# Kernel tuning notes

Hardware: AMD Instinct MI355X
Metric: run time of the kernel (lower is better)

The kernel has to match this reference:

```python
import jax, jax.numpy as jnp
import numpy as np
from jax import lax

B, N_CELL, N_NODE, E, H = 512, 12, 40, 128, 128
CLIP = 10.0
NEG = -1e9


def _ptr_logits(query, target, mask, Wq, bq, Wk, bk, v):
    # query [B,E], target [B,N,E], mask [B,N] (1 = visited)
    u = jnp.einsum('bnh,h->bn', jnp.tanh((query @ Wq + bq)[:, None, :] + target @ Wk + bk), v)
    return jnp.where(mask > 0, NEG, CLIP * jnp.tanh(u))


def _forward(node_context, cell_context, original_data, high_mask, low_mask,
             init_w, W_hc, b_hc, W_vw, b_vw, Wq, bq, Wk, bk, v,
             low_init_w, low_W_hc, low_b_hc, low_W_vw, low_b_vw,
             low_Wq, low_bq, low_Wk, low_bk, low_v):
    ar = jnp.arange(B)
    root = jax.random.key(42)
    high_keys = jax.random.split(jax.random.fold_in(root, 0), N_CELL)
    low_keys = jax.random.split(jax.random.fold_in(root, 1), N_CELL)

    def low_decode(cell_emb, cell_coords, key):
        # cell_emb [B,n_node,E], cell_coords [B,n_node,2]
        h_bar = jnp.mean(cell_emb, 1) @ low_W_hc + low_b_hc
        q0 = h_bar + low_init_w @ low_W_vw + low_b_vw

        def step(carry, k):
            query, mask, init_h, i = carry
            logits = _ptr_logits(query, cell_emb, mask, low_Wq, low_bq, low_Wk, low_bk, low_v)
            idx = jax.random.categorical(k, logits)            # [B]
            lp = jnp.take_along_axis(jax.nn.log_softmax(logits, -1), idx[:, None], 1)[:, 0]
            mask = mask.at[ar, idx].set(1.0)
            h = cell_emb[ar, idx]
            coord = cell_coords[ar, idx]
            init_h = jnp.where(i == 0, h, init_h)
            query = h_bar + jnp.concatenate([init_h, h], -1) @ low_W_vw + low_b_vw
            return (query, mask, init_h, i + 1), (idx, lp, coord)

        keys = jax.random.split(key, N_NODE)
        carry0 = (q0, low_mask, jnp.zeros_like(h_bar), jnp.int32(0))
        _, (idxs, lps, coords) = lax.scan(step, carry0, keys)
        # tour length inside the cell
        reward = jnp.sum(jnp.linalg.norm(coords[1:] - coords[:-1], axis=-1), 0)  # [B]
        return lps.sum(0), idxs.T, reward, coords[0], coords[-1]

    h_bar = jnp.mean(cell_context, 1) @ W_hc + b_hc
    q0 = h_bar + init_w @ W_vw + b_vw

    def step(carry, ks):
        query, mask, init_h, last_node, i = carry
        k_hi, k_lo = ks
        logits = _ptr_logits(query, cell_context, mask, Wq, bq, Wk, bk, v)
        idx = jax.random.categorical(k_hi, logits)             # [B]
        clp = jnp.take_along_axis(jax.nn.log_softmax(logits, -1), idx[:, None], 1)[:, 0]
        cur_emb = node_context[ar, idx]                        # [B,n_node,E]
        cur_coords = original_data[ar, idx]                    # [B,n_node,2]
        llp, lact, lrew, init_node, new_last = low_decode(cur_emb, cur_coords, k_lo)
        # distance from previous cell's last node to this cell's first node (i>0 only)
        crew = jnp.where(i > 0, jnp.linalg.norm(init_node - last_node, axis=1), 0.0)
        mask = mask.at[ar, idx].set(1.0)
        h = cell_context[ar, idx]
        init_h = jnp.where(i == 0, h, init_h)
        query = h_bar + jnp.concatenate([init_h, h], -1) @ W_vw + b_vw
        return (query, mask, init_h, new_last, i + 1), (idx, clp, crew, llp, lact, lrew)

    carry0 = (q0, high_mask, jnp.zeros_like(h_bar), jnp.zeros((B, 2), jnp.float32), jnp.int32(0))
    _, (idxs, clps, crews, llps, lacts, lrews) = lax.scan(step, carry0, (high_keys, low_keys))

    cell_log_prob = clps.sum(0)                                # [B]
    cell_action = idxs.T                                       # [B, n_cell]
    cell_reward = crews.sum(0)                                 # [B] (i==0 term is 0)
    node_log_prob = llps.T.reshape(-1, 1)                      # [B*n_cell, 1]
    node_action = jnp.transpose(lacts, (1, 0, 2)).reshape(-1, N_NODE)
    node_reward = lrews.T.reshape(-1, 1)
    return cell_log_prob, node_log_prob, cell_reward, node_reward, cell_action, node_action


def setup_inputs() -> dict:
    key = jax.random.key(0)
    ks = jax.random.split(key, 32)

    def lin(k, fan_in, shape):
        b = 1.0 / np.sqrt(fan_in)
        return jax.random.uniform(k, shape, jnp.float32, -b, b)

    return {
        'node_context': jax.random.normal(ks[0], (B, N_CELL, N_NODE, E), jnp.float32),
        'cell_context': jax.random.normal(ks[1], (B, N_CELL, E), jnp.float32),
        'original_data': jax.random.uniform(ks[2], (B, N_CELL, N_NODE, 2), jnp.float32),
        'high_mask': jnp.zeros((B, N_CELL), jnp.float32),
        'low_mask': jnp.zeros((B, N_NODE), jnp.float32),
        'init_w': jax.random.uniform(ks[3], (2 * E,), jnp.float32, -1.0, 1.0),
        'W_hc': lin(ks[4], E, (E, E)), 'b_hc': lin(ks[5], E, (E,)),
        'W_vw': lin(ks[6], 2 * E, (2 * E, E)), 'b_vw': lin(ks[7], 2 * E, (E,)),
        'Wq': lin(ks[8], E, (E, H)), 'bq': lin(ks[9], E, (H,)),
        'Wk': lin(ks[10], E, (E, H)), 'bk': lin(ks[11], E, (H,)),
        'v': lin(ks[12], H, (H,)),
        'low_init_w': jax.random.uniform(ks[13], (2 * E,), jnp.float32, -1.0, 1.0),
        'low_W_hc': lin(ks[14], E, (E, E)), 'low_b_hc': lin(ks[15], E, (E,)),
        'low_W_vw': lin(ks[16], 2 * E, (2 * E, E)), 'low_b_vw': lin(ks[17], 2 * E, (E,)),
        'low_Wq': lin(ks[18], E, (E, H)), 'low_bq': lin(ks[19], E, (H,)),
        'low_Wk': lin(ks[20], E, (E, H)), 'low_bk': lin(ks[21], E, (H,)),
        'low_v': lin(ks[22], H, (H,)),
    }


def reference(node_context, cell_context, original_data, high_mask, low_mask,
              init_w, W_hc, b_hc, W_vw, b_vw, Wq, bq, Wk, bk, v,
              low_init_w, low_W_hc, low_b_hc, low_W_vw, low_b_vw,
              low_Wq, low_bq, low_Wk, low_bk, low_v):
    return _forward(node_context, cell_context, original_data, high_mask, low_mask,
                    init_w, W_hc, b_hc, W_vw, b_vw, Wq, bq, Wk, bk, v,
                    low_init_w, low_W_hc, low_b_hc, low_W_vw, low_b_vw,
                    low_Wq, low_bq, low_Wk, low_bk, low_v)
```

## Files before the change

kernel.cpp:

```cpp
#include <hip/hip_runtime.h>
#include <stdint.h>


#define NB    512
#define NCELL 12
#define NNODE 40
#define EDIM  128
#define EDP   129
#define THREADS 256

#define OFF_CLP  0
#define OFF_NLP  512
#define OFF_CRW  6656
#define OFF_NRW  7168
#define OFF_CACT 13312
#define OFF_NACT 19456

#define WS_PTS_BASE   6144
#define WS_META_BASE  30720
#define WS_U_BASE     55296
#define WS_GUM_BASE   9885696
#define WS_TOTAL_F    19716096ull

__device__ __forceinline__ uint32_t rotl32(uint32_t x, int d) {
  return (x << d) | (x >> (32 - d));
}

__device__ __forceinline__ void tf2x32(uint32_t k0, uint32_t k1,
                                       uint32_t c0, uint32_t c1,
                                       uint32_t& o0, uint32_t& o1) {
  uint32_t ks2 = k0 ^ k1 ^ 0x1BD11BDAu;
  uint32_t x0 = c0 + k0, x1 = c1 + k1;
#define TFR(r) { x0 += x1; x1 = rotl32(x1, (r)); x1 ^= x0; }
  TFR(13) TFR(15) TFR(26) TFR(6)   x0 += k1;  x1 += ks2 + 1u;
  TFR(17) TFR(29) TFR(16) TFR(24)  x0 += ks2; x1 += k0 + 2u;
  TFR(13) TFR(15) TFR(26) TFR(6)   x0 += k0;  x1 += k1 + 3u;
  TFR(17) TFR(29) TFR(16) TFR(24)  x0 += k1;  x1 += ks2 + 4u;
  TFR(13) TFR(15) TFR(26) TFR(6)   x0 += ks2; x1 += k0 + 5u;
#undef TFR
  o0 = x0; o1 = x1;
}

__device__ __forceinline__ uint32_t draw_bits(uint32_t k0, uint32_t k1,
                                              uint32_t idx) {
  uint32_t o0, o1;
  tf2x32(k0, k1, 0u, idx, o0, o1);
  return o0 ^ o1;
}

__device__ __forceinline__ float bits_to_gumbel(uint32_t bits) {
  uint32_t fb = (bits >> 9) | 0x3F800000u;
  float f = __uint_as_float(fb) - 1.0f;
  const float TINY = 1.17549435082228751e-38f;
  float u = f * (1.0f - TINY) + TINY;
  u = fmaxf(TINY, u);
  return -logf(-logf(u));
}

__device__ __forceinline__ float xla_tanh(float x) {
#pragma clang fp contract(off)
  float ax = fabsf(x);
  float xc = fminf(fmaxf(x, -9.0f), 9.0f);
  float x2 = xc * xc;
  float nm = -2.76076847742355e-16f;
  nm = nm * x2 + 2.00018790482477e-13f;
  nm = nm * x2 + -8.60467152213735e-11f;
  nm = nm * x2 + 5.12229709037114e-08f;
  nm = nm * x2 + 1.48572235717979e-05f;
  nm = nm * x2 + 6.37261928875436e-04f;
  nm = nm * x2 + 4.89352455891786e-03f;
  nm = xc * nm;
  float dn = 1.19825839466702e-06f;
  dn = dn * x2 + 1.18534705686654e-04f;
  dn = dn * x2 + 2.26843463243900e-03f;
  dn = dn * x2 + 4.89352518554385e-03f;
  return (ax < 0.0004f) ? x : (nm / dn);
}

template<int KLEN>
__device__ __forceinline__ void matvec(const float* __restrict__ W,
                                       const float* __restrict__ src,
                                       const float* __restrict__ pre,
                                       const float* __restrict__ bias,
                                       float* dest, float* part, int t) {
  const int j  = t & 127;
  const int hv = t >> 7;
  const int kh = KLEN / 2;
  const int k0 = hv * kh;
  float acc = 0.f;
  const float* Wp = W + (size_t)k0 * EDIM + j;
  const float* sp = src + k0;
#pragma unroll 8
  for (int k = 0; k < kh; ++k) acc = fmaf(sp[k], Wp[(size_t)k * EDIM], acc);
  if (hv) part[j] = acc;
  __syncthreads();
  if (!hv) {
    float r = acc + part[j];
    if (pre)  r += pre[j];
    if (bias) r += bias[j];
    dest[j] = r;
  }
  __syncthreads();
}

template<int RPH, int SSTR, int DSTR>
__device__ __forceinline__ void computeK(const float* __restrict__ W,
                                         const float* __restrict__ bias,
                                         const float* src, float* dst, int t) {
  const int j  = t & 127;
  const int hv = t >> 7;
  float acc[RPH];
#pragma unroll
  for (int s = 0; s < RPH; ++s) acc[s] = 0.f;
  const float* Wp = W + j;
#pragma unroll 4
  for (int k = 0; k < EDIM; ++k) {
    float w = Wp[(size_t)k * EDIM];
#pragma unroll
    for (int s = 0; s < RPH; ++s)
      acc[s] = fmaf(src[(hv + 2 * s) * SSTR + k], w, acc[s]);
  }
  float bj = bias[j];
#pragma unroll
  for (int s = 0; s < RPH; ++s) dst[(hv + 2 * s) * DSTR + j] = acc[s] + bj;
}

__global__ __launch_bounds__(THREADS, 2)
void high_kernel(const float* __restrict__ cell_context,
                 const float* __restrict__ high_mask,
                 const float* __restrict__ init_w,
                 const float* __restrict__ W_hc,  const float* __restrict__ b_hc,
                 const float* __restrict__ W_vw,  const float* __restrict__ b_vw,
                 const float* __restrict__ Wq,    const float* __restrict__ bq,
                 const float* __restrict__ Wk,    const float* __restrict__ bk,
                 const float* __restrict__ v_hi,
                 float* __restrict__ out, int* __restrict__ ws_cidx) {
  const int b = blockIdx.x;
  const int t = threadIdx.x;

  __shared__ float s_cc[NCELL][EDIM];
  __shared__ float s_Kh[NCELL][EDIM];
  __shared__ float s_ghum[NCELL * NCELL];
  __shared__ float s_qh[EDIM], s_qq[EDIM], s_qbh[EDIM], s_hbh[EDIM];
  __shared__ float s_mean[EDIM], s_part[EDIM];
  __shared__ float s_vh[EDIM], s_bqh[EDIM];
  __shared__ float s_iw[2 * EDIM];
  __shared__ float s_u[NCELL];
  __shared__ float s_maskh[NCELL];
  __shared__ uint32_t s_kh[NCELL][2];
  __shared__ uint32_t s_base[2];
  __shared__ int s_idx;

  if (t == 0) {
    uint32_t a0, a1;
    tf2x32(0u, 42u, 0u, 0u, a0, a1); s_base[0] = a0; s_base[1] = a1;
  }
  __syncthreads();
  if (t < NCELL)
    tf2x32(s_base[0], s_base[1], 0u, (uint32_t)t, s_kh[t][0], s_kh[t][1]);

  if (t < EDIM) { s_vh[t] = v_hi[t]; s_bqh[t] = bq[t]; }
  s_iw[t] = init_w[t];
  if (t < NCELL) s_maskh[t] = high_mask[b * NCELL + t];

  if (t < EDIM) {
    float s = 0.f;
    for (int n = 0; n < NCELL; ++n) {
      float x = cell_context[((size_t)b * NCELL + n) * EDIM + t];
      s_cc[n][t] = x; s += x;
    }
    s_mean[t] = s / 12.0f;
  }
  __syncthreads();
  if (t < NCELL * NCELL) {
    int ci = t / NCELL, n = t - ci * NCELL;
    s_ghum[t] = bits_to_gumbel(draw_bits(s_kh[ci][0], s_kh[ci][1],
                                         (uint32_t)(b * NCELL + n)));
  }
  matvec<128>(W_hc, s_mean, nullptr, b_hc, s_hbh, s_part, t);
  computeK<6, EDIM, EDIM>(Wk, bk, &s_cc[0][0], &s_Kh[0][0], t);
  __syncthreads();
  matvec<256>(W_vw, s_iw, s_hbh, b_vw, s_qh, s_part, t);
  if (t < EDIM) s_qbh[t] = s_hbh[t] + b_vw[t];
  __syncthreads();

  float cell_lp = 0.f;

  for (int ci = 0; ci < NCELL; ++ci) {
    matvec<128>(Wq, s_qh, nullptr, s_bqh, s_qq, s_part, t);
    if (t < 4 * NCELL) {
      int nd = t >> 2, p = t & 3, rot = t & 31;
      float acc = 0.f;
#pragma unroll 4
      for (int i2 = 0; i2 < 32; ++i2) {
        int h = p * 32 + ((i2 + rot) & 31);
        acc = fmaf(s_vh[h], xla_tanh(s_qq[h] + s_Kh[nd][h]), acc);
      }
      acc += __shfl_xor(acc, 1);
      acc += __shfl_xor(acc, 2);
      if (p == 0) s_u[nd] = acc;
    }
    __syncthreads();

    if (t < 64) {
      float logit = -__builtin_huge_valf(), val = -__builtin_huge_valf();
      if (t < NCELL) {
        float lg = (s_maskh[t] > 0.f) ? -1e9f : 10.0f * xla_tanh(s_u[t]);
        logit = lg;
        val = lg + s_ghum[ci * NCELL + t];
      }
      int bidx = t;
      float mx = logit;
#pragma unroll
      for (int d = 32; d; d >>= 1) {
        float oval = __shfl_xor(val, d);
        int   oidx = __shfl_xor(bidx, d);
        float omx  = __shfl_xor(mx, d);
        if (oval > val || (oval == val && oidx < bidx)) { val = oval; bidx = oidx; }
        mx = fmaxf(mx, omx);
      }
      float ex = (t < NCELL) ? expf(logit - mx) : 0.f;
#pragma unroll
      for (int d = 32; d; d >>= 1) ex += __shfl_xor(ex, d);
      float chosen = __shfl(logit, bidx);
      cell_lp += (chosen - mx) - logf(ex);
      if (t == 0) {
        s_idx = bidx;
        s_maskh[bidx] = 1.0f;
        out[OFF_CACT + b * NCELL + ci] = (float)bidx;
        ws_cidx[b * NCELL + ci] = bidx;
      }
    }
    __syncthreads();
    const int cidx = s_idx;

    if (ci == 0)
      matvec<128>(W_vw, &s_cc[cidx][0], s_qbh, nullptr, s_qbh, s_part, t);
    if (ci < NCELL - 1)
      matvec<128>(W_vw + 128 * EDIM, &s_cc[cidx][0], s_qbh, nullptr, s_qh, s_part, t);
  }

  if (t == 0) out[OFF_CLP + b] = cell_lp;
}

__global__ __launch_bounds__(THREADS, 3)
void low_pre_kernel(const float* __restrict__ node_context,
                    const float* __restrict__ original_data,
                    const float* __restrict__ low_mask,
                    const float* __restrict__ low_init_w,
                    const float* __restrict__ low_W_hc, const float* __restrict__ low_b_hc,
                    const float* __restrict__ low_W_vw, const float* __restrict__ low_b_vw,
                    const float* __restrict__ low_Wq,   const float* __restrict__ low_bq,
                    const float* __restrict__ low_Wk,   const float* __restrict__ low_bk,
                    const float* __restrict__ v_lo,
                    const int* __restrict__ ws_cidx,
                    float* __restrict__ ws_meta,
                    float* __restrict__ ws_U,
                    float* __restrict__ ws_gum,
                    float* __restrict__ out) {
  const int bc = blockIdx.x;
  const int b  = bc / NCELL;
  const int ci = bc - b * NCELL;
  const int t  = threadIdx.x;
  const int j  = t & 127;
  const int hv = t >> 7;

  __shared__ float s_eq[NNODE * EDP];
  __shared__ float s_Kl[NNODE * EDP];
  __shared__ float s_g0[NNODE];
  __shared__ float s_coords[NNODE][2];
  __shared__ float s_ql[EDIM], s_qq[EDIM], s_qbl[EDIM], s_hbl[EDIM];
  __shared__ float s_mean[EDIM], s_part[EDIM];
  __shared__ float s_vl[EDIM], s_bql[EDIM];
  __shared__ float s_iwl[2 * EDIM];
  __shared__ float s_u[NNODE];
  __shared__ float s_maskl[NNODE];
  __shared__ uint32_t s_ks[NNODE][2];
  __shared__ uint32_t s_kk[2];
  __shared__ int s_cidx;
  __shared__ int s_idx;

  if (t == 0) {
    uint32_t a0, a1, c0, c1;
    tf2x32(0u, 42u, 0u, 1u, a0, a1);
    tf2x32(a0, a1, 0u, (uint32_t)ci, c0, c1);
    s_kk[0] = c0; s_kk[1] = c1;
    s_cidx = ws_cidx[bc];
  }
  __syncthreads();
  const int cidx = s_cidx;

  if (t < EDIM) { s_vl[t] = v_lo[t]; s_bql[t] = low_bq[t]; }
  s_iwl[t] = low_init_w[t];
  if (t < NNODE)
    tf2x32(s_kk[0], s_kk[1], 0u, (uint32_t)t, s_ks[t][0], s_ks[t][1]);

  const float* embg = node_context + (((size_t)b * NCELL + cidx) * NNODE) * EDIM;
  if (t < EDIM) {
    float s = 0.f;
    for (int n = 0; n < NNODE; ++n) {
      float x = embg[n * EDIM + t];
      s_eq[n * EDP + t] = x; s += x;
    }
    s_mean[t] = s / 40.0f;
  }
  if (t >= 128 && t < 208) {
    int q = t - 128;
    s_coords[q >> 1][q & 1] = original_data[(((size_t)b * NCELL + cidx) * NNODE) * 2 + q];
  }
  if (t >= 208 && t < 208 + NNODE) s_maskl[t - 208] = low_mask[b * NNODE + (t - 208)];
  __syncthreads();

  {
    float* gg = ws_gum + (size_t)bc * (NNODE * NNODE);
    for (int g = t; g < NNODE * NNODE; g += THREADS) {
      int st = g / NNODE, n = g - st * NNODE;
      float gv = bits_to_gumbel(draw_bits(s_ks[st][0], s_ks[st][1],
                                          (uint32_t)(b * NNODE + n)));
      gg[g] = gv;
      if (g < NNODE) s_g0[g] = gv;
    }
  }
  matvec<128>(low_W_hc, s_mean, nullptr, low_b_hc, s_hbl, s_part, t);
  computeK<20, EDP, EDP>(low_Wk, low_bk, &s_eq[0], &s_Kl[0], t);

  {
    float accA[20], accB[20];
#pragma unroll
    for (int s = 0; s < 20; ++s) { accA[s] = 0.f; accB[s] = 0.f; }
    const float* Wb = low_W_vw + (size_t)128 * EDIM + j;
#pragma unroll 2
    for (int k = 0; k < 64; ++k) {
      float w = Wb[(size_t)k * EDIM];
#pragma unroll
      for (int s = 0; s < 20; ++s)
        accA[s] = fmaf(s_eq[(hv + 2 * s) * EDP + k], w, accA[s]);
    }
#pragma unroll 2
    for (int k = 64; k < 128; ++k) {
      float w = Wb[(size_t)k * EDIM];
#pragma unroll
      for (int s = 0; s < 20; ++s)
        accB[s] = fmaf(s_eq[(hv + 2 * s) * EDP + k], w, accB[s]);
    }
    __syncthreads();
#pragma unroll
    for (int s = 0; s < 20; ++s)
      s_eq[(hv + 2 * s) * EDP + j] = accA[s] + accB[s];
  }
  matvec<256>(low_W_vw, s_iwl, s_hbl, low_b_vw, s_ql, s_part, t);
  if (t < EDIM) s_qbl[t] = s_hbl[t] + low_b_vw[t];
  __syncthreads();

  matvec<128>(low_Wq, s_ql, nullptr, s_bql, s_qq, s_part, t);
  if (t < 160) {
    int nd = t >> 2, p = t & 3, rot = t & 31;
    float acc = 0.f;
#pragma unroll 4
    for (int i2 = 0; i2 < 32; ++i2) {
      int h = p * 32 + ((i2 + rot) & 31);
      acc = fmaf(s_vl[h], xla_tanh(s_qq[h] + s_Kl[nd * EDP + h]), acc);
    }
    acc += __shfl_xor(acc, 1);
    acc += __shfl_xor(acc, 2);
    if (p == 0) s_u[nd] = acc;
  }
  __syncthreads();

  if (t < 64) {
    float maskreg = (t < NNODE) ? s_maskl[t] : 1.0f;
    float logit = -__builtin_huge_valf(), val = -__builtin_huge_valf();
    if (t < NNODE) {
      float lg = (maskreg > 0.f) ? -1e9f : 10.0f * xla_tanh(s_u[t]);
      logit = lg;
      val = lg + s_g0[t];
    }
    int bidx = t;
    float mx = logit;
#pragma unroll
    for (int d = 32; d; d >>= 1) {
      float oval = __shfl_xor(val, d);
      int   oidx = __shfl_xor(bidx, d);
      float omx  = __shfl_xor(mx, d);
      if (oval > val || (oval == val && oidx < bidx)) { val = oval; bidx = oidx; }
      mx = fmaxf(mx, omx);
    }
    float ex = (t < NNODE) ? expf(logit - mx) : 0.f;
#pragma unroll
    for (int d = 32; d; d >>= 1) ex += __shfl_xor(ex, d);
    float chosen = __shfl(logit, bidx);
    float lp0 = (chosen - mx) - logf(ex);
    if (t == 0) {
      s_idx = bidx;
      out[OFF_NACT + ((size_t)bc) * NNODE + 0] = (float)bidx;
      float4 m; m.x = s_coords[bidx][0]; m.y = s_coords[bidx][1];
      m.z = lp0; m.w = (float)bidx;
      reinterpret_cast<float4*>(ws_meta)[bc] = m;
    }
  }
  __syncthreads();

  {
    const int n0 = s_idx;
    matvec<128>(low_W_vw, embg + (size_t)n0 * EDIM, s_qbl, nullptr, s_qbl, s_part, t);
    for (int i = t; i < NNODE * EDIM; i += THREADS) {
      int n = i >> 7, k = i & 127;
      s_eq[n * EDP + k] = s_eq[n * EDP + k] + s_qbl[k];
    }
    __syncthreads();
    {
      float ac0[20], ac1[20];
#pragma unroll
      for (int s = 0; s < 20; ++s) { ac0[s] = 0.f; ac1[s] = 0.f; }
      const float* Wqp = low_Wq + (size_t)(hv * 64) * EDIM + j;
      const float* qlb = &s_eq[0] + hv * 64;
#pragma unroll 2
      for (int k = 0; k < 64; ++k) {
        float w = Wqp[(size_t)k * EDIM];
#pragma unroll
        for (int s = 0; s < 20; ++s)
          ac0[s] = fmaf(qlb[s * EDP + k], w, ac0[s]);
#pragma unroll
        for (int s = 0; s < 20; ++s)
          ac1[s] = fmaf(qlb[(20 + s) * EDP + k], w, ac1[s]);
      }
      __syncthreads();
      if (hv) {
#pragma unroll
        for (int s = 0; s < 20; ++s) {
          s_eq[s * EDP + j]        = ac0[s];
          s_eq[(20 + s) * EDP + j] = ac1[s];
        }
      }
      __syncthreads();
      if (!hv) {
#pragma unroll
        for (int s = 0; s < 20; ++s) {
          s_eq[s * EDP + j]        = (ac0[s] + s_eq[s * EDP + j])        + s_bql[j];
          s_eq[(20 + s) * EDP + j] = (ac1[s] + s_eq[(20 + s) * EDP + j]) + s_bql[j];
        }
      }
      __syncthreads();
    }
  }

  {
    float* wU = ws_U + (size_t)bc * (NNODE * NNODE);
    for (int e = t; e < NNODE * NNODE; e += THREADS) {
      int nd = e / NNODE, prow = e - nd * NNODE;
      const float* qr = &s_eq[prow * EDP];
      const float* kr = &s_Kl[nd * EDP];
      float S[4];
#pragma unroll
      for (int p = 0; p < 4; ++p) {
        int rot = (4 * nd + p) & 31;
        float a = 0.f;
#pragma unroll 4
        for (int i2 = 0; i2 < 32; ++i2) {
          int h = p * 32 + ((i2 + rot) & 31);
          a = fmaf(s_vl[h], xla_tanh(qr[h] + kr[h]), a);
        }
        S[p] = a;
      }
      wU[prow * NNODE + nd] = (S[0] + S[1]) + (S[2] + S[3]);
    }
  }
}

__global__ __launch_bounds__(64)
void low_tail_kernel(const float* __restrict__ original_data,
                     const float* __restrict__ low_mask,
                     const int* __restrict__ ws_cidx,
                     const float* __restrict__ ws_meta,
                     const float* __restrict__ ws_U,
                     const float* __restrict__ ws_gum,
                     float* __restrict__ ws_pts,
                     float* __restrict__ out) {
  const int bc = blockIdx.x;
  const int b  = bc / NCELL;
  const int t  = threadIdx.x;

  __shared__ float sU[NNODE * NNODE];
  __shared__ float sG[NNODE * NNODE];
  __shared__ float sc[NNODE][2];
  __shared__ int s_cidx;

  if (t == 0) s_cidx = ws_cidx[bc];
  __syncthreads();
  const int cidx = s_cidx;

  {
    const float4* u4 = reinterpret_cast<const float4*>(ws_U + (size_t)bc * 1600);
    const float4* g4 = reinterpret_cast<const float4*>(ws_gum + (size_t)bc * 1600);
    float4* su4 = reinterpret_cast<float4*>(sU);
    float4* sg4 = reinterpret_cast<float4*>(sG);
    for (int i = t; i < 400; i += 64) { su4[i] = u4[i]; sg4[i] = g4[i]; }
    for (int q = t; q < 80; q += 64)
      sc[q >> 1][q & 1] = original_data[(((size_t)b * NCELL + cidx) * NNODE) * 2 + q];
  }
  float4 meta = reinterpret_cast<const float4*>(ws_meta)[bc];
  int   prev  = (int)meta.w;
  float initx = meta.x, inity = meta.y;
  float llp   = meta.z;
  float prevx = initx, prevy = inity, rew = 0.f;
  float maskreg = (t < NNODE) ? low_mask[b * NNODE + t] : 1.0f;
  if (t == prev) maskreg = 1.0f;
  __syncthreads();

  for (int st = 1; st < NNODE; ++st) {
    float logit = -__builtin_huge_valf(), val = -__builtin_huge_valf();
    if (t < NNODE) {
      float lg = (maskreg > 0.f) ? -1e9f : 10.0f * xla_tanh(sU[prev * NNODE + t]);
      logit = lg;
      val = lg + sG[st * NNODE + t];
    }
    int bidx = t;
    float mx = logit;
#pragma unroll
    for (int d = 32; d; d >>= 1) {
      float oval = __shfl_xor(val, d);
      int   oidx = __shfl_xor(bidx, d);
      float omx  = __shfl_xor(mx, d);
      if (oval > val || (oval == val && oidx < bidx)) { val = oval; bidx = oidx; }
      mx = fmaxf(mx, omx);
    }
    float ex = (t < NNODE) ? expf(logit - mx) : 0.f;
#pragma unroll
    for (int d = 32; d; d >>= 1) ex += __shfl_xor(ex, d);
    float chosen = __shfl(logit, bidx);
    llp += (chosen - mx) - logf(ex);
    float cx = sc[bidx][0], cy = sc[bidx][1];
    { float dx = cx - prevx, dy = cy - prevy; rew += sqrtf(dx * dx + dy * dy); }
    prevx = cx; prevy = cy;
    if (t == bidx) maskreg = 1.0f;
    prev = bidx;
    if (t == 0)
      out[OFF_NACT + ((size_t)bc) * NNODE + st] = (float)bidx;
  }
  if (t == 0) {
    out[OFF_NLP + bc] = llp;
    out[OFF_NRW + bc] = rew;
    float* p = ws_pts + (size_t)bc * 4;
    p[0] = initx; p[1] = inity; p[2] = prevx; p[3] = prevy;
  }
}

__global__ __launch_bounds__(THREADS, 2)
void low_kernel_fused(const float* __restrict__ node_context,
                      const float* __restrict__ original_data,
                      const float* __restrict__ low_mask,
                      const float* __restrict__ low_init_w,
                      const float* __restrict__ low_W_hc, const float* __restrict__ low_b_hc,
                      const float* __restrict__ low_W_vw, const float* __restrict__ low_b_vw,
                      const float* __restrict__ low_Wq,   const float* __restrict__ low_bq,
                      const float* __restrict__ low_Wk,   const float* __restrict__ low_bk,
                      const float* __restrict__ v_lo,
                      const int* __restrict__ ws_cidx,
                      float* __restrict__ ws_pts,
                      float* __restrict__ out) {
  const int bc = blockIdx.x;
  const int b  = bc / NCELL;
  const int ci = bc - b * NCELL;
  const int t  = threadIdx.x;
  const int j  = t & 127;
  const int hv = t >> 7;

  __shared__ float s_eq[NNODE * EDP];
  __shared__ float s_Kl[NNODE * EDP];
  __shared__ float s_U[NNODE * NNODE];
  __shared__ float s_gum[NNODE * NNODE];
  __shared__ float s_coords[NNODE][2];
  __shared__ float s_ql[EDIM], s_qq[EDIM], s_qbl[EDIM], s_hbl[EDIM];
  __shared__ float s_mean[EDIM], s_part[EDIM];
  __shared__ float s_vl[EDIM], s_bql[EDIM];
  __shared__ float s_iwl[2 * EDIM];
  __shared__ float s_u[NNODE];
  __shared__ float s_maskl[NNODE];
  __shared__ uint32_t s_ks[NNODE][2];
  __shared__ uint32_t s_kk[2];
  __shared__ int s_cidx;
  __shared__ int s_idx;

  if (t == 0) {
    uint32_t a0, a1, c0, c1;
    tf2x32(0u, 42u, 0u, 1u, a0, a1);
    tf2x32(a0, a1, 0u, (uint32_t)ci, c0, c1);
    s_kk[0] = c0; s_kk[1] = c1;
    s_cidx = ws_cidx[bc];
  }
  __syncthreads();
  const int cidx = s_cidx;

  if (t < EDIM) { s_vl[t] = v_lo[t]; s_bql[t] = low_bq[t]; }
  s_iwl[t] = low_init_w[t];
  if (t < NNODE)
    tf2x32(s_kk[0], s_kk[1], 0u, (uint32_t)t, s_ks[t][0], s_ks[t][1]);

  const float* embg = node_context + (((size_t)b * NCELL + cidx) * NNODE) * EDIM;
  if (t < EDIM) {
    float s = 0.f;
    for (int n = 0; n < NNODE; ++n) {
      float x = embg[n * EDIM + t];
      s_eq[n * EDP + t] = x; s += x;
    }
    s_mean[t] = s / 40.0f;
  }
  if (t >= 128 && t < 208) {
    int q = t - 128;
    s_coords[q >> 1][q & 1] = original_data[(((size_t)b * NCELL + cidx) * NNODE) * 2 + q];
  }
  if (t >= 208 && t < 208 + NNODE) s_maskl[t - 208] = low_mask[b * NNODE + (t - 208)];
  __syncthreads();

  for (int g = t; g < NNODE * NNODE; g += THREADS) {
    int st = g / NNODE, n = g - st * NNODE;
    s_gum[g] = bits_to_gumbel(draw_bits(s_ks[st][0], s_ks[st][1],
                                        (uint32_t)(b * NNODE + n)));
  }
  matvec<128>(low_W_hc, s_mean, nullptr, low_b_hc, s_hbl, s_part, t);
  computeK<20, EDP, EDP>(low_Wk, low_bk, &s_eq[0], &s_Kl[0], t);

  {
    float accA[20], accB[20];
#pragma unroll
    for (int s = 0; s < 20; ++s) { accA[s] = 0.f; accB[s] = 0.f; }
    const float* Wb = low_W_vw + (size_t)128 * EDIM + j;
#pragma unroll 2
    for (int k = 0; k < 64; ++k) {
      float w = Wb[(size_t)k * EDIM];
#pragma unroll
      for (int s = 0; s < 20; ++s)
        accA[s] = fmaf(s_eq[(hv + 2 * s) * EDP + k], w, accA[s]);
    }
#pragma unroll 2
    for (int k = 64; k < 128; ++k) {
      float w = Wb[(size_t)k * EDIM];
#pragma unroll
      for (int s = 0; s < 20; ++s)
        accB[s] = fmaf(s_eq[(hv + 2 * s) * EDP + k], w, accB[s]);
    }
    __syncthreads();
#pragma unroll
    for (int s = 0; s < 20; ++s)
      s_eq[(hv + 2 * s) * EDP + j] = accA[s] + accB[s];
  }
  matvec<256>(low_W_vw, s_iwl, s_hbl, low_b_vw, s_ql, s_part, t);
  if (t < EDIM) s_qbl[t] = s_hbl[t] + low_b_vw[t];
  __syncthreads();

  matvec<128>(low_Wq, s_ql, nullptr, s_bql, s_qq, s_part, t);
  if (t < 160) {
    int nd = t >> 2, p = t & 3, rot = t & 31;
    float acc = 0.f;
#pragma unroll 4
    for (int i2 = 0; i2 < 32; ++i2) {
      int h = p * 32 + ((i2 + rot) & 31);
      acc = fmaf(s_vl[h], xla_tanh(s_qq[h] + s_Kl[nd * EDP + h]), acc);
    }
    acc += __shfl_xor(acc, 1);
    acc += __shfl_xor(acc, 2);
    if (p == 0) s_u[nd] = acc;
  }
  __syncthreads();

  float llp = 0.f, rew = 0.f, prevx = 0.f, prevy = 0.f, initx = 0.f, inity = 0.f;
  float maskreg = 1.0f;
  int prev = 0;
  if (t < 64) {
    maskreg = (t < NNODE) ? s_maskl[t] : 1.0f;
    float logit = -__builtin_huge_valf(), val = -__builtin_huge_valf();
    if (t < NNODE) {
      float lg = (maskreg > 0.f) ? -1e9f : 10.0f * xla_tanh(s_u[t]);
      logit = lg;
      val = lg + s_gum[t];
    }
    int bidx = t;
    float mx = logit;
#pragma unroll
    for (int d = 32; d; d >>= 1) {
      float oval = __shfl_xor(val, d);
      int   oidx = __shfl_xor(bidx, d);
      float omx  = __shfl_xor(mx, d);
      if (oval > val || (oval == val && oidx < bidx)) { val = oval; bidx = oidx; }
      mx = fmaxf(mx, omx);
    }
    float ex = (t < NNODE) ? expf(logit - mx) : 0.f;
#pragma unroll
    for (int d = 32; d; d >>= 1) ex += __shfl_xor(ex, d);
    float chosen = __shfl(logit, bidx);
    llp += (chosen - mx) - logf(ex);
    initx = s_coords[bidx][0]; inity = s_coords[bidx][1];
    prevx = initx; prevy = inity;
    if (t == bidx) maskreg = 1.0f;
    prev = bidx;
    if (t == 0) {
      s_idx = bidx;
      out[OFF_NACT + ((size_t)bc) * NNODE + 0] = (float)bidx;
    }
  }
  __syncthreads();

  {
    const int n0 = s_idx;
    matvec<128>(low_W_vw, embg + (size_t)n0 * EDIM, s_qbl, nullptr, s_qbl, s_part, t);
    for (int i = t; i < NNODE * EDIM; i += THREADS) {
      int n = i >> 7, k = i & 127;
      s_eq[n * EDP + k] = s_eq[n * EDP + k] + s_qbl[k];
    }
    __syncthreads();
    {
      float ac0[20], ac1[20];
#pragma unroll
      for (int s = 0; s < 20; ++s) { ac0[s] = 0.f; ac1[s] = 0.f; }
      const float* Wqp = low_Wq + (size_t)(hv * 64) * EDIM + j;
      const float* qlb = &s_eq[0] + hv * 64;
#pragma unroll 2
      for (int k = 0; k < 64; ++k) {
        float w = Wqp[(size_t)k * EDIM];
#pragma unroll
        for (int s = 0; s < 20; ++s)
          ac0[s] = fmaf(qlb[s * EDP + k], w, ac0[s]);
#pragma unroll
        for (int s = 0; s < 20; ++s)
          ac1[s] = fmaf(qlb[(20 + s) * EDP + k], w, ac1[s]);
      }
      __syncthreads();
      if (hv) {
#pragma unroll
        for (int s = 0; s < 20; ++s) {
          s_eq[s * EDP + j]        = ac0[s];
          s_eq[(20 + s) * EDP + j] = ac1[s];
        }
      }
      __syncthreads();
      if (!hv) {
#pragma unroll
        for (int s = 0; s < 20; ++s) {
          s_eq[s * EDP + j]        = (ac0[s] + s_eq[s * EDP + j])        + s_bql[j];
          s_eq[(20 + s) * EDP + j] = (ac1[s] + s_eq[(20 + s) * EDP + j]) + s_bql[j];
        }
      }
      __syncthreads();
    }
  }

  for (int e = t; e < NNODE * NNODE; e += THREADS) {
    int nd = e / NNODE, prow = e - nd * NNODE;
    const float* qr = &s_eq[prow * EDP];
    const float* kr = &s_Kl[nd * EDP];
    float S[4];
#pragma unroll
    for (int p = 0; p < 4; ++p) {
      int rot = (4 * nd + p) & 31;
      float a = 0.f;
#pragma unroll 4
      for (int i2 = 0; i2 < 32; ++i2) {
        int h = p * 32 + ((i2 + rot) & 31);
        a = fmaf(s_vl[h], xla_tanh(qr[h] + kr[h]), a);
      }
      S[p] = a;
    }
    s_U[prow * NNODE + nd] = (S[0] + S[1]) + (S[2] + S[3]);
  }
  __syncthreads();

  if (t < 64) {
    for (int st = 1; st < NNODE; ++st) {
      float logit = -__builtin_huge_valf(), val = -__builtin_huge_valf();
      if (t < NNODE) {
        float lg = (maskreg > 0.f) ? -1e9f : 10.0f * xla_tanh(s_U[prev * NNODE + t]);
        logit = lg;
        val = lg + s_gum[st * NNODE + t];
      }
      int bidx = t;
      float mx = logit;
#pragma unroll
      for (int d = 32; d; d >>= 1) {
        float oval = __shfl_xor(val, d);
        int   oidx = __shfl_xor(bidx, d);
        float omx  = __shfl_xor(mx, d);
        if (oval > val || (oval == val && oidx < bidx)) { val = oval; bidx = oidx; }
        mx = fmaxf(mx, omx);
      }
      float ex = (t < NNODE) ? expf(logit - mx) : 0.f;
#pragma unroll
      for (int d = 32; d; d >>= 1) ex += __shfl_xor(ex, d);
      float chosen = __shfl(logit, bidx);
      llp += (chosen - mx) - logf(ex);
      float cx = s_coords[bidx][0], cy = s_coords[bidx][1];
      { float dx = cx - prevx, dy = cy - prevy; rew += sqrtf(dx * dx + dy * dy); }
      prevx = cx; prevy = cy;
      if (t == bidx) maskreg = 1.0f;
      prev = bidx;
      if (t == 0)
        out[OFF_NACT + ((size_t)bc) * NNODE + st] = (float)bidx;
    }
    if (t == 0) {
      out[OFF_NLP + bc] = llp;
      out[OFF_NRW + bc] = rew;
      float* p = ws_pts + (size_t)bc * 4;
      p[0] = initx; p[1] = inity; p[2] = prevx; p[3] = prevy;
    }
  }
}

__global__ void link_kernel(const float* __restrict__ ws_pts,
                            float* __restrict__ out) {
  int b = blockIdx.x * blockDim.x + threadIdx.x;
  if (b >= NB) return;
  float crew = 0.f;
  for (int ci = 1; ci < NCELL; ++ci) {
    const float* cur = ws_pts + (size_t)(b * NCELL + ci) * 4;
    const float* prv = ws_pts + (size_t)(b * NCELL + ci - 1) * 4;
    float dx = cur[0] - prv[2], dy = cur[1] - prv[3];
    crew += sqrtf(dx * dx + dy * dy);
  }
  out[OFF_CRW + b] = crew;
}

extern "C" void kernel_launch(void* const* d_in, const int* in_sizes, int n_in,
                              void* d_out, int out_size, void* d_ws, size_t ws_size,
                              hipStream_t stream) {
  (void)in_sizes; (void)n_in; (void)out_size;
  const float* node_context  = (const float*)d_in[0];
  const float* cell_context  = (const float*)d_in[1];
  const float* original_data = (const float*)d_in[2];
  const float* high_mask     = (const float*)d_in[3];
  const float* low_mask      = (const float*)d_in[4];
  const float* init_w        = (const float*)d_in[5];
  const float* W_hc  = (const float*)d_in[6];
  const float* b_hc  = (const float*)d_in[7];
  const float* W_vw  = (const float*)d_in[8];
  const float* b_vw  = (const float*)d_in[9];
  const float* Wq    = (const float*)d_in[10];
  const float* bq    = (const float*)d_in[11];
  const float* Wk    = (const float*)d_in[12];
  const float* bk    = (const float*)d_in[13];
  const float* v_hi  = (const float*)d_in[14];
  const float* low_init_w = (const float*)d_in[15];
  const float* low_W_hc   = (const float*)d_in[16];
  const float* low_b_hc   = (const float*)d_in[17];
  const float* low_W_vw   = (const float*)d_in[18];
  const float* low_b_vw   = (const float*)d_in[19];
  const float* low_Wq     = (const float*)d_in[20];
  const float* low_bq     = (const float*)d_in[21];
  const float* low_Wk     = (const float*)d_in[22];
  const float* low_bk     = (const float*)d_in[23];
  const float* v_lo       = (const float*)d_in[24];
  float* out = (float*)d_out;
  float* wsf = (float*)d_ws;
  int*   ws_cidx = (int*)d_ws;
  float* ws_pts  = wsf + WS_PTS_BASE;
  float* ws_meta = wsf + WS_META_BASE;
  float* ws_U    = wsf + WS_U_BASE;
  float* ws_gum  = wsf + WS_GUM_BASE;

  high_kernel<<<NB, THREADS, 0, stream>>>(
      cell_context, high_mask, init_w, W_hc, b_hc, W_vw, b_vw,
      Wq, bq, Wk, bk, v_hi, out, ws_cidx);

  if (ws_size >= WS_TOTAL_F * 4ull) {
    low_pre_kernel<<<NB * NCELL, THREADS, 0, stream>>>(
        node_context, original_data, low_mask, low_init_w,
        low_W_hc, low_b_hc, low_W_vw, low_b_vw,
        low_Wq, low_bq, low_Wk, low_bk, v_lo,
        ws_cidx, ws_meta, ws_U, ws_gum, out);
    low_tail_kernel<<<NB * NCELL, 64, 0, stream>>>(
        original_data, low_mask, ws_cidx, ws_meta, ws_U, ws_gum, ws_pts, out);
  } else {
    low_kernel_fused<<<NB * NCELL, THREADS, 0, stream>>>(
        node_context, original_data, low_mask, low_init_w,
        low_W_hc, low_b_hc, low_W_vw, low_b_vw,
        low_Wq, low_bq, low_Wk, low_bk, v_lo,
        ws_cidx, ws_pts, out);
  }

  link_kernel<<<2, 256, 0, stream>>>(ws_pts, out);
}
```

Measured before the change: 2.121 ms.

## Generate low-level Gumbel noise in extra high_kernel blocks; split rotated tanh loop

Moves the per-cell Gumbel noise generation out of low_pre_kernel into extra blocks appended to the high_kernel launch, so it runs alongside the sequential high-level decode instead of on the low_pre critical path. low_pre_kernel now just reads its first row of noise from the workspace. The rotated U-score loop is also split into two contiguous ranges to drop the per-iteration modulo indexing. The catch is a larger high_kernel grid, and the extra blocks still allocate the high path's shared memory.

```diff
diff --git a/kernel.cpp b/kernel.cpp
--- a/kernel.cpp
+++ b/kernel.cpp
@@ -134,8 +134,8 @@
                  const float* __restrict__ Wq,    const float* __restrict__ bq,
                  const float* __restrict__ Wk,    const float* __restrict__ bk,
                  const float* __restrict__ v_hi,
-                 float* __restrict__ out, int* __restrict__ ws_cidx) {
-  const int b = blockIdx.x;
+                 float* __restrict__ out, int* __restrict__ ws_cidx,
+                 float* __restrict__ ws_gum) {
   const int t = threadIdx.x;
 
   __shared__ float s_cc[NCELL][EDIM];
@@ -149,7 +149,29 @@
   __shared__ float s_maskh[NCELL];
   __shared__ uint32_t s_kh[NCELL][2];
   __shared__ uint32_t s_base[2];
+  __shared__ uint32_t g_ks[NNODE][2];
   __shared__ int s_idx;
+
+  if (blockIdx.x >= NB) {
+    const int bc = blockIdx.x - NB;
+    const int b  = bc / NCELL;
+    const int ci = bc - b * NCELL;
+    uint32_t a0, a1, c0, c1;
+    tf2x32(0u, 42u, 0u, 1u, a0, a1);
+    tf2x32(a0, a1, 0u, (uint32_t)ci, c0, c1);
+    if (t < NNODE)
+      tf2x32(c0, c1, 0u, (uint32_t)t, g_ks[t][0], g_ks[t][1]);
+    __syncthreads();
+    float* gg = ws_gum + (size_t)bc * (NNODE * NNODE);
+    for (int g = t; g < NNODE * NNODE; g += THREADS) {
+      int st = g / NNODE, n = g - st * NNODE;
+      gg[g] = bits_to_gumbel(draw_bits(g_ks[st][0], g_ks[st][1],
+                                       (uint32_t)(b * NNODE + n)));
+    }
+    return;
+  }
+
+  const int b = blockIdx.x;
 
   if (t == 0) {
     uint32_t a0, a1;
@@ -256,11 +278,10 @@
                     const int* __restrict__ ws_cidx,
                     float* __restrict__ ws_meta,
                     float* __restrict__ ws_U,
-                    float* __restrict__ ws_gum,
+                    const float* __restrict__ ws_gum,
                     float* __restrict__ out) {
   const int bc = blockIdx.x;
   const int b  = bc / NCELL;
-  const int ci = bc - b * NCELL;
   const int t  = threadIdx.x;
   const int j  = t & 127;
   const int hv = t >> 7;
@@ -275,25 +296,16 @@
   __shared__ float s_iwl[2 * EDIM];
   __shared__ float s_u[NNODE];
   __shared__ float s_maskl[NNODE];
-  __shared__ uint32_t s_ks[NNODE][2];
-  __shared__ uint32_t s_kk[2];
   __shared__ int s_cidx;
   __shared__ int s_idx;
 
-  if (t == 0) {
-    uint32_t a0, a1, c0, c1;
-    tf2x32(0u, 42u, 0u, 1u, a0, a1);
-    tf2x32(a0, a1, 0u, (uint32_t)ci, c0, c1);
-    s_kk[0] = c0; s_kk[1] = c1;
-    s_cidx = ws_cidx[bc];
-  }
+  if (t == 0) s_cidx = ws_cidx[bc];
   __syncthreads();
   const int cidx = s_cidx;
 
   if (t < EDIM) { s_vl[t] = v_lo[t]; s_bql[t] = low_bq[t]; }
   s_iwl[t] = low_init_w[t];
-  if (t < NNODE)
-    tf2x32(s_kk[0], s_kk[1], 0u, (uint32_t)t, s_ks[t][0], s_ks[t][1]);
+  if (t < NNODE) s_g0[t] = ws_gum[(size_t)bc * (NNODE * NNODE) + t];
 
   const float* embg = node_context + (((size_t)b * NCELL + cidx) * NNODE) * EDIM;
   if (t < EDIM) {
@@ -311,16 +323,6 @@
   if (t >= 208 && t < 208 + NNODE) s_maskl[t - 208] = low_mask[b * NNODE + (t - 208)];
   __syncthreads();
 
-  {
-    float* gg = ws_gum + (size_t)bc * (NNODE * NNODE);
-    for (int g = t; g < NNODE * NNODE; g += THREADS) {
-      int st = g / NNODE, n = g - st * NNODE;
-      float gv = bits_to_gumbel(draw_bits(s_ks[st][0], s_ks[st][1],
-                                          (uint32_t)(b * NNODE + n)));
-      gg[g] = gv;
-      if (g < NNODE) s_g0[g] = gv;
-    }
-  }
   matvec<128>(low_W_hc, s_mean, nullptr, low_b_hc, s_hbl, s_part, t);
   computeK<20, EDP, EDP>(low_Wk, low_bk, &s_eq[0], &s_Kl[0], t);
 
@@ -453,13 +455,17 @@
       float S[4];
 #pragma unroll
       for (int p = 0; p < 4; ++p) {
-        int rot = (4 * nd + p) & 31;
+        const int rot = (4 * nd + p) & 31;
+        const float* aq = qr + p * 32;
+        const float* ak = kr + p * 32;
+        const float* av = s_vl + p * 32;
         float a = 0.f;
 #pragma unroll 4
-        for (int i2 = 0; i2 < 32; ++i2) {
-          int h = p * 32 + ((i2 + rot) & 31);
-          a = fmaf(s_vl[h], xla_tanh(qr[h] + kr[h]), a);
-        }
+        for (int h = rot; h < 32; ++h)
+          a = fmaf(av[h], xla_tanh(aq[h] + ak[h]), a);
+#pragma unroll 4
+        for (int h = 0; h < rot; ++h)
+          a = fmaf(av[h], xla_tanh(aq[h] + ak[h]), a);
         S[p] = a;
       }
       wU[prow * NNODE + nd] = (S[0] + S[1]) + (S[2] + S[3]);
@@ -855,11 +861,13 @@
   float* ws_U    = wsf + WS_U_BASE;
   float* ws_gum  = wsf + WS_GUM_BASE;
 
-  high_kernel<<<NB, THREADS, 0, stream>>>(
+  const bool big_ws = (ws_size >= WS_TOTAL_F * 4ull);
+
+  high_kernel<<<big_ws ? (NB + NB * NCELL) : NB, THREADS, 0, stream>>>(
       cell_context, high_mask, init_w, W_hc, b_hc, W_vw, b_vw,
-      Wq, bq, Wk, bk, v_hi, out, ws_cidx);
-
-  if (ws_size >= WS_TOTAL_F * 4ull) {
+      Wq, bq, Wk, bk, v_hi, out, ws_cidx, ws_gum);
+
+  if (big_ws) {
     low_pre_kernel<<<NB * NCELL, THREADS, 0, stream>>>(
         node_context, original_data, low_mask, low_init_w,
         low_W_hc, low_b_hc, low_W_vw, low_b_vw,
```

Result: slower. 2.196 ms (+3.5%).
